# Kernel optimization log

Hardware: AMD Instinct MI355X
Metric: run time of the kernel (lower is better)

Reference implementation:

```python
import jax, jax.numpy as jnp
import numpy as np

N, H, W = 4, 96, 96
C, G, K = 128, 8, 3
GC = C // G          # group channels = 16
P = K * K            # sampling points per group = 9
PAD = K // 2
OFS = 1.0            # offset_scale
HID = 4 * C          # mlp hidden
EPS = 1e-5           # torch nn.LayerNorm default eps


def _ln(x, g, b):
    m = jnp.mean(x, -1, keepdims=True)
    v = jnp.mean((x - m) ** 2, -1, keepdims=True)
    return (x - m) * jax.lax.rsqrt(v + EPS) * g + b


def _dcnv3_core(x, offset, mask):
    # x: (n,H,W,C) channels-last, offset: (n,H,W,G*P*2), mask: (n,H,W,G,P) softmaxed.
    # Faithful port of dcnv3_core_pytorch (stride=1, dilation=1, zero-pad grid_sample,
    # align_corners=False -> pixel = loc*size - 0.5).
    n = x.shape[0]
    xp = jnp.pad(x, ((0, 0), (PAD, PAD), (PAD, PAD), (0, 0)))
    Hin, Win = H + 2 * PAD, W + 2 * PAD
    L = H * W
    base = (K - 1) // 2 + 0.5
    ref_x = (base + jnp.arange(W, dtype=x.dtype)) / Win  # normalized by padded size
    ref_y = (base + jnp.arange(H, dtype=x.dtype)) / Hin
    k = jnp.arange(K, dtype=x.dtype) - (K - 1) // 2
    dx = jnp.repeat(k, K) / Win  # torch meshgrid('ij'): kernel-x varies slowest
    dy = jnp.tile(k, K) / Hin
    off = offset.reshape(n, H, W, G, P, 2)
    # absolute sampling pixel coords (grid_sample align_corners=False)
    px = (ref_x[None, None, :, None, None] + dx * OFS + off[..., 0] * OFS / Win) * Win - 0.5
    py = (ref_y[None, :, None, None, None] + dy * OFS + off[..., 1] * OFS / Hin) * Hin - 0.5
    # layout (n,G,L,P)
    px = px.transpose(0, 3, 1, 2, 4).reshape(n, G, L, P)
    py = py.transpose(0, 3, 1, 2, 4).reshape(n, G, L, P)
    mk = mask.transpose(0, 3, 1, 2, 4).reshape(n, G, L, P)
    xg = xp.reshape(n, Hin * Win, G, GC).transpose(0, 2, 1, 3)
    x0 = jnp.floor(px); y0 = jnp.floor(py)
    fx = px - x0; fy = py - y0
    x0 = x0.astype(jnp.int32); y0 = y0.astype(jnp.int32)
    x1 = x0 + 1; y1 = y0 + 1
    out = jnp.zeros((n, G, L, GC), x.dtype)
    for yi, xi, w in ((y0, x0, (1 - fy) * (1 - fx)), (y0, x1, (1 - fy) * fx),
                      (y1, x0, fy * (1 - fx)), (y1, x1, fy * fx)):
        valid = (yi >= 0) & (yi < Hin) & (xi >= 0) & (xi < Win)
        idx = jnp.clip(yi, 0, Hin - 1) * Win + jnp.clip(xi, 0, Win - 1)
        v = jnp.take_along_axis(xg, idx.reshape(n, G, L * P, 1), axis=2)
        v = v.reshape(n, G, L, P, GC)
        out = out + jnp.einsum('nglp,nglpc->nglc', jnp.where(valid, w, 0.0) * mk, v)
    return out.transpose(0, 2, 1, 3).reshape(n, H, W, C)


def _dcn(x, w_in, b_in, dw_k, dw_b, dwg, dwb, w_off, b_off, w_msk, b_msk, w_out, b_out):
    n = x.shape[0]
    xproj = x @ w_in + b_in
    x1 = jax.lax.conv_general_dilated(
        x, dw_k, (1, 1), 'SAME',
        dimension_numbers=('NHWC', 'HWIO', 'NHWC'),
        feature_group_count=C) + dw_b
    x1 = jax.nn.gelu(_ln(x1, dwg, dwb), approximate=False)
    offset = x1 @ w_off + b_off
    mask = jax.nn.softmax((x1 @ w_msk + b_msk).reshape(n, H, W, G, P), axis=-1)
    y = _dcnv3_core(xproj, offset, mask)
    return y @ w_out + b_out


def setup_inputs() -> dict:
    key = jax.random.key(0)
    ks = jax.random.split(key, 10)
    rn = lambda k, s, sc: jax.random.normal(k, s, jnp.float32) * sc
    return {
        'x': rn(ks[0], (N, H, W, C), 1.0),
        'ln1g': jnp.ones((C,), jnp.float32), 'ln1b': jnp.zeros((C,), jnp.float32),
        'w_in': rn(ks[1], (C, C), 0.02), 'b_in': jnp.zeros((C,), jnp.float32),
        'dw_k': rn(ks[2], (K, K, 1, C), 0.1), 'dw_b': jnp.zeros((C,), jnp.float32),
        'dwg': jnp.ones((C,), jnp.float32), 'dwb': jnp.zeros((C,), jnp.float32),
        'w_off': rn(ks[3], (C, G * P * 2), 0.01), 'b_off': rn(ks[4], (G * P * 2,), 0.1),
        'w_msk': rn(ks[5], (C, G * P), 0.02), 'b_msk': jnp.zeros((G * P,), jnp.float32),
        'w_out': rn(ks[6], (C, C), 0.02), 'b_out': jnp.zeros((C,), jnp.float32),
        'ln2g': jnp.ones((C,), jnp.float32), 'ln2b': jnp.zeros((C,), jnp.float32),
        'w1': rn(ks[7], (C, HID), 0.02), 'b1': jnp.zeros((HID,), jnp.float32),
        'w2': rn(ks[8], (HID, C), 0.02), 'b2': jnp.zeros((C,), jnp.float32),
    }


def reference(x, ln1g, ln1b, w_in, b_in, dw_k, dw_b, dwg, dwb, w_off, b_off,
              w_msk, b_msk, w_out, b_out, ln2g, ln2b, w1, b1, w2, b2):
    # pre-norm InternImage block: x = x + dcn(LN1(x)); x = x + mlp(LN2(x))
    x = x + _dcn(_ln(x, ln1g, ln1b), w_in, b_in, dw_k, dw_b, dwg, dwb,
                 w_off, b_off, w_msk, b_msk, w_out, b_out)
    h = _ln(x, ln2g, ln2b)
    h = jax.nn.gelu(h @ w1 + b1, approximate=False) @ w2 + b2
    return x + h
```

## Files before the change

kernel.cpp:

```cpp
#include <hip/hip_runtime.h>
#include <hip/hip_bf16.h>
#include <math.h>

using bf16 = __hip_bfloat16;
using bf162 = __hip_bfloat162;

typedef __bf16 bf16x8 __attribute__((ext_vector_type(8)));
typedef float floatx4 __attribute__((ext_vector_type(4)));

constexpr int NB = 4, HH = 96, WW = 96, CC = 128, GG = 8, PP = 9;
constexpr int HW = HH * WW;
constexpr int NPIX = NB * HW;

__device__ __forceinline__ float ld1(const float* p) { return *p; }
__device__ __forceinline__ float ld1(const bf16* p)  { return __bfloat162float(*p); }
__device__ __forceinline__ void st1(float* p, float v) { *p = v; }
__device__ __forceinline__ void st1(bf16* p, float v)  { *p = __float2bfloat16(v); }
__device__ __forceinline__ float b2f(bf16 v) { return __bfloat162float(v); }
__device__ __forceinline__ bf16 f2b(float v) { return __float2bfloat16(v); }
__device__ __forceinline__ float gelu_exact(float v) {
    return 0.5f * v * (1.0f + erff(v * 0.7071067811865475f));
}
__device__ __forceinline__ floatx4 MFMA(bf16x8 a, bf16x8 b, floatx4 c) {
    return __builtin_amdgcn_mfma_f32_16x16x32_bf16(a, b, c, 0, 0, 0);
}

struct PrepArgs {
    const float* src[6];
    bf16* dst[6];
    int K[6], N[6];
    int cum[7];
    const float* b_off; const float* b_msk; float* b_om;
};

__global__ __launch_bounds__(256) void prep_weights(PrepArgs pa, int total)
{
    int t = blockIdx.x * 256 + threadIdx.x;
    if (t >= total) return;
    if (t >= pa.cum[6]) {
        int e = t - pa.cum[6];
        pa.b_om[e] = (e < 144) ? pa.b_off[e] : pa.b_msk[e - 144];
        return;
    }
    int i = 0;
    #pragma unroll
    for (int j = 0; j < 5; ++j) if (t >= pa.cum[j + 1]) i = j + 1;
    int e = t - pa.cum[i];
    int Ki = pa.K[i], Ni = pa.N[i];
    int n = e / Ki, k = e - n * Ki;
    pa.dst[i][e] = f2b(pa.src[i][(size_t)k * Ni + n]);
}

template<typename TI, typename TO>
__global__ __launch_bounds__(256) void ln_kernel(
    const TI* __restrict__ X, const float* __restrict__ g,
    const float* __restrict__ b, TO* __restrict__ out)
{
    int wave = (blockIdx.x * 256 + threadIdx.x) >> 6;
    int lane = threadIdx.x & 63;
    if (wave >= NPIX) return;
    const TI* xp = X + (size_t)wave * 128 + 2 * lane;
    float v0 = ld1(xp), v1 = ld1(xp + 1);
    float s = v0 + v1, q = v0 * v0 + v1 * v1;
    #pragma unroll
    for (int o = 32; o; o >>= 1) { s += __shfl_xor(s, o); q += __shfl_xor(q, o); }
    float mean = s * (1.0f / 128.0f);
    float rstd = rsqrtf(q * (1.0f / 128.0f) - mean * mean + 1e-5f);
    float g0 = g[2 * lane], g1 = g[2 * lane + 1];
    float b0 = b[2 * lane], b1 = b[2 * lane + 1];
    TO* op = out + (size_t)wave * 128 + 2 * lane;
    st1(op,     (v0 - mean) * rstd * g0 + b0);
    st1(op + 1, (v1 - mean) * rstd * g1 + b1);
}

__global__ __launch_bounds__(256) void dwconv_ln_gelu_kernel(
    const bf16* __restrict__ xln, const float* __restrict__ dwk,
    const float* __restrict__ dwb, const float* __restrict__ gam,
    const float* __restrict__ bet, bf16* __restrict__ out)
{
    int wave = (blockIdx.x * 256 + threadIdx.x) >> 6;
    int lane = threadIdx.x & 63;
    if (wave >= NPIX) return;
    int n = wave / HW; int rem = wave % HW;
    int y = rem / WW;  int x = rem % WW;
    const bf162* xp = (const bf162*)xln;
    float a0 = 0.f, a1 = 0.f;
    #pragma unroll
    for (int ky = 0; ky < 3; ++ky) {
        int yy = y + ky - 1;
        if (yy < 0 || yy >= HH) continue;
        #pragma unroll
        for (int kx = 0; kx < 3; ++kx) {
            int xx = x + kx - 1;
            if (xx < 0 || xx >= WW) continue;
            bf162 v = xp[((size_t)(n * HH + yy) * WW + xx) * 64 + lane];
            const float* w = dwk + (ky * 3 + kx) * CC + 2 * lane;
            a0 = fmaf(b2f(v.x), w[0], a0);
            a1 = fmaf(b2f(v.y), w[1], a1);
        }
    }
    a0 += dwb[2 * lane]; a1 += dwb[2 * lane + 1];
    float s = a0 + a1, q = a0 * a0 + a1 * a1;
    #pragma unroll
    for (int o = 32; o; o >>= 1) { s += __shfl_xor(s, o); q += __shfl_xor(q, o); }
    float mean = s * (1.0f / 128.0f);
    float rstd = rsqrtf(q * (1.0f / 128.0f) - mean * mean + 1e-5f);
    float h0 = gelu_exact((a0 - mean) * rstd * gam[2 * lane]     + bet[2 * lane]);
    float h1 = gelu_exact((a1 - mean) * rstd * gam[2 * lane + 1] + bet[2 * lane + 1]);
    bf162 o2; o2.x = f2b(h0); o2.y = f2b(h1);
    ((bf162*)out)[(size_t)wave * 64 + lane] = o2;
}

__global__ __launch_bounds__(256) void dcn_core_kernel(
    const bf16* __restrict__ xproj, const bf16* __restrict__ omr,
    bf16* __restrict__ out)
{
    __shared__ int4   sOff[4][72];
    __shared__ float4 sW[4][72];
    __shared__ float  sRaw[4][72];
    int wv = threadIdx.x >> 6;
    int lane = threadIdx.x & 63;
    int pix = blockIdx.x * 4 + wv;
    int n = pix / HW; int rem = pix % HW;
    int iy = rem / WW; int ix = rem % WW;
    const bf16* om = omr + (size_t)pix * 216;

    for (int e = lane; e < 72; e += 64)
        sRaw[wv][e] = b2f(om[144 + e]);
    __syncthreads();

    for (int e = lane; e < 72; e += 64) {
        int g = e / 9, p = e - 9 * g;
        float mx = -1e30f;
        #pragma unroll
        for (int i = 0; i < 9; ++i) mx = fmaxf(mx, sRaw[wv][g * 9 + i]);
        float ssum = 0.f;
        #pragma unroll
        for (int i = 0; i < 9; ++i) ssum += __expf(sRaw[wv][g * 9 + i] - mx);
        float mw = __expf(sRaw[wv][e] - mx) / ssum;

        float ox = b2f(om[g * 18 + 2 * p]);
        float oy = b2f(om[g * 18 + 2 * p + 1]);
        int kx = p / 3 - 1, ky = p % 3 - 1;
        float px = (float)(ix + kx) + ox;
        float py = (float)(iy + ky) + oy;
        float fx0 = floorf(px), fy0 = floorf(py);
        int x0 = (int)fx0, y0 = (int)fy0;
        float fx = px - fx0, fy = py - fy0;
        bool vx0 = (x0 >= 0) & (x0 < WW), vx1 = (x0 + 1 >= 0) & (x0 + 1 < WW);
        bool vy0 = (y0 >= 0) & (y0 < HH), vy1 = (y0 + 1 >= 0) & (y0 + 1 < HH);
        float w00 = (1.f - fy) * (1.f - fx) * mw * (vy0 && vx0 ? 1.f : 0.f);
        float w01 = (1.f - fy) * fx         * mw * (vy0 && vx1 ? 1.f : 0.f);
        float w10 = fy * (1.f - fx)         * mw * (vy1 && vx0 ? 1.f : 0.f);
        float w11 = fy * fx                 * mw * (vy1 && vx1 ? 1.f : 0.f);
        int x0c = min(max(x0, 0), WW - 1), x1c = min(max(x0 + 1, 0), WW - 1);
        int y0c = min(max(y0, 0), HH - 1), y1c = min(max(y0 + 1, 0), HH - 1);
        sOff[wv][e] = make_int4((y0c * WW + x0c) * CC, (y0c * WW + x1c) * CC,
                                (y1c * WW + x0c) * CC, (y1c * WW + x1c) * CC);
        sW[wv][e] = make_float4(w00, w01, w10, w11);
    }
    __syncthreads();

    const bf16* xb = xproj + (size_t)n * HW * CC + 2 * lane;
    int gbase = (lane >> 3) * 9;
    float a0 = 0.f, a1 = 0.f;
    #pragma unroll
    for (int p = 0; p < 9; ++p) {
        int4 o = sOff[wv][gbase + p];
        float4 w = sW[wv][gbase + p];
        bf162 v00 = *(const bf162*)(xb + o.x);
        bf162 v01 = *(const bf162*)(xb + o.y);
        bf162 v10 = *(const bf162*)(xb + o.z);
        bf162 v11 = *(const bf162*)(xb + o.w);
        a0 += w.x * b2f(v00.x) + w.y * b2f(v01.x) + w.z * b2f(v10.x) + w.w * b2f(v11.x);
        a1 += w.x * b2f(v00.y) + w.y * b2f(v01.y) + w.z * b2f(v10.y) + w.w * b2f(v11.y);
    }
    bf162 o2; o2.x = f2b(a0); o2.y = f2b(a1);
    ((bf162*)out)[(size_t)pix * 64 + lane] = o2;
}

__global__ __launch_bounds__(256) void gemm_mfma_kernel(
    const bf16* __restrict__ A, const bf16* __restrict__ Wt,
    const float* __restrict__ bias, bf16* __restrict__ Out, int M, int Nn)
{
    __shared__ __align__(16) __bf16 As[64][136];
    __shared__ __align__(16) __bf16 Bs[64][136];
    int tid = threadIdx.x;
    int wv = tid >> 6, lane = tid & 63;
    int bm = blockIdx.y * 64, bn = blockIdx.x * 64;
    int mI = lane & 15, q = lane >> 4;

    #pragma unroll
    for (int i = 0; i < 4; ++i) {
        int s = tid + 256 * i;
        int row = s >> 4, ko = (s & 15) * 8;
        *reinterpret_cast<uint4*>(&As[row][ko]) =
            *reinterpret_cast<const uint4*>(A + (size_t)(bm + row) * 128 + ko);
        int ng = bn + row;
        uint4 bv = make_uint4(0, 0, 0, 0);
        if (ng < Nn) bv = *reinterpret_cast<const uint4*>(Wt + (size_t)ng * 128 + ko);
        *reinterpret_cast<uint4*>(&Bs[row][ko]) = bv;
    }
    __syncthreads();

    floatx4 acc[4] = {};
    #pragma unroll
    for (int ks = 0; ks < 4; ++ks) {
        int k = ks * 32 + q * 8;
        bf16x8 a = *reinterpret_cast<const bf16x8*>(&As[wv * 16 + mI][k]);
        #pragma unroll
        for (int t = 0; t < 4; ++t) {
            bf16x8 b = *reinterpret_cast<const bf16x8*>(&Bs[t * 16 + mI][k]);
            acc[t] = MFMA(a, b, acc[t]);
        }
    }
    int row0 = bm + wv * 16 + q * 4;
    #pragma unroll
    for (int t = 0; t < 4; ++t) {
        int col = bn + t * 16 + mI;
        if (col >= Nn) continue;
        float bs = bias[col];
        #pragma unroll
        for (int r = 0; r < 4; ++r)
            st1(Out + (size_t)(row0 + r) * Nn + col, acc[t][r] + bs);
    }
}

__global__ __launch_bounds__(256, 3) void fused_tail_kernel(
    const bf16* __restrict__ ycore, const float* __restrict__ x,
    const bf16* __restrict__ w_outT, const float* __restrict__ b_out,
    const float* __restrict__ ln2g, const float* __restrict__ ln2b,
    const bf16* __restrict__ w1T, const float* __restrict__ b1,
    const bf16* __restrict__ w2T, const float* __restrict__ b2,
    float* __restrict__ out)
{
    __shared__ __align__(16) bf16 sA[64 * 136];
    __shared__ __align__(16) bf16 sXres[64 * 136];
    __shared__ __align__(16) bf16 sH2[64 * 136];
    int tid = threadIdx.x, wv = tid >> 6, lane = tid & 63;
    int mI = lane & 15, q = lane >> 4;
    int bm = blockIdx.x * 64;

    bf16x8 bw0[4][2];
    #pragma unroll
    for (int ks = 0; ks < 4; ++ks)
        #pragma unroll
        for (int ct = 0; ct < 2; ++ct)
            bw0[ks][ct] = *reinterpret_cast<const bf16x8*>(
                w_outT + (size_t)(wv * 32 + ct * 16 + mI) * 128 + ks * 32 + q * 8);

    #pragma unroll
    for (int i = 0; i < 4; ++i) {
        int s = tid + 256 * i;
        int row = s >> 4, ko = (s & 15) * 8;
        *reinterpret_cast<uint4*>(&sA[row * 136 + ko]) =
            *reinterpret_cast<const uint4*>(ycore + (size_t)(bm + row) * 128 + ko);
    }
    __syncthreads();

    floatx4 acc0[4][2] = {};
    #pragma unroll
    for (int ks = 0; ks < 4; ++ks) {
        int k = ks * 32 + q * 8;
        bf16x8 a[4];
        #pragma unroll
        for (int rt = 0; rt < 4; ++rt)
            a[rt] = *reinterpret_cast<const bf16x8*>(&sA[(rt * 16 + mI) * 136 + k]);
        #pragma unroll
        for (int ct = 0; ct < 2; ++ct)
            #pragma unroll
            for (int rt = 0; rt < 4; ++rt)
                acc0[rt][ct] = MFMA(a[rt], bw0[ks][ct], acc0[rt][ct]);
    }
    #pragma unroll
    for (int rt = 0; rt < 4; ++rt)
        #pragma unroll
        for (int ct = 0; ct < 2; ++ct) {
            int col = wv * 32 + ct * 16 + mI;
            float bs = b_out[col];
            #pragma unroll
            for (int r = 0; r < 4; ++r) {
                int row = rt * 16 + q * 4 + r;
                float v = acc0[rt][ct][r] + bs + x[(size_t)(bm + row) * 128 + col];
                sXres[row * 136 + col] = f2b(v);
            }
        }
    __syncthreads();

    {
        int row = tid >> 2, part = tid & 3;
        float s = 0.f, sq = 0.f;
        float vals[32];
        #pragma unroll
        for (int j = 0; j < 4; ++j) {
            bf16x8 v = *reinterpret_cast<const bf16x8*>(&sXres[row * 136 + part * 32 + j * 8]);
            #pragma unroll
            for (int e = 0; e < 8; ++e) {
                float f = (float)v[e];
                vals[j * 8 + e] = f; s += f; sq += f * f;
            }
        }
        s  += __shfl_xor(s, 1);  s += __shfl_xor(s, 2);
        sq += __shfl_xor(sq, 1); sq += __shfl_xor(sq, 2);
        float mean = s * (1.0f / 128.0f);
        float rstd = rsqrtf(sq * (1.0f / 128.0f) - mean * mean + 1e-5f);
        #pragma unroll
        for (int j = 0; j < 4; ++j) {
            bf16x8 o;
            #pragma unroll
            for (int e = 0; e < 8; ++e) {
                int ch = part * 32 + j * 8 + e;
                bf16 t = f2b((vals[j * 8 + e] - mean) * rstd * ln2g[ch] + ln2b[ch]);
                o[e] = *reinterpret_cast<__bf16*>(&t);
            }
            *reinterpret_cast<bf16x8*>(&sH2[row * 136 + part * 32 + j * 8]) = o;
        }
    }
    __syncthreads();

    floatx4 acc2[4][2] = {};
    #pragma unroll 1
    for (int ph = 0; ph < 4; ++ph) {
        bf16x8 bw1[4][2];
        #pragma unroll
        for (int ks = 0; ks < 4; ++ks)
            #pragma unroll
            for (int ct = 0; ct < 2; ++ct)
                bw1[ks][ct] = *reinterpret_cast<const bf16x8*>(
                    w1T + (size_t)(ph * 128 + wv * 32 + ct * 16 + mI) * 128 + ks * 32 + q * 8);
        floatx4 acc1[4][2] = {};
        #pragma unroll
        for (int ks = 0; ks < 4; ++ks) {
            int k = ks * 32 + q * 8;
            bf16x8 a[4];
            #pragma unroll
            for (int rt = 0; rt < 4; ++rt)
                a[rt] = *reinterpret_cast<const bf16x8*>(&sH2[(rt * 16 + mI) * 136 + k]);
            #pragma unroll
            for (int ct = 0; ct < 2; ++ct)
                #pragma unroll
                for (int rt = 0; rt < 4; ++rt)
                    acc1[rt][ct] = MFMA(a[rt], bw1[ks][ct], acc1[rt][ct]);
        }
        __syncthreads();
        bf16x8 bw2[4][2];
        #pragma unroll
        for (int ks = 0; ks < 4; ++ks)
            #pragma unroll
            for (int ct = 0; ct < 2; ++ct)
                bw2[ks][ct] = *reinterpret_cast<const bf16x8*>(
                    w2T + (size_t)(wv * 32 + ct * 16 + mI) * 512 + ph * 128 + ks * 32 + q * 8);
        #pragma unroll
        for (int rt = 0; rt < 4; ++rt)
            #pragma unroll
            for (int ct = 0; ct < 2; ++ct) {
                int lcol = wv * 32 + ct * 16 + mI;
                float bs = b1[ph * 128 + lcol];
                #pragma unroll
                for (int r = 0; r < 4; ++r) {
                    int row = rt * 16 + q * 4 + r;
                    sA[row * 136 + lcol] = f2b(gelu_exact(acc1[rt][ct][r] + bs));
                }
            }
        __syncthreads();
        #pragma unroll
        for (int ks = 0; ks < 4; ++ks) {
            int k = ks * 32 + q * 8;
            bf16x8 a[4];
            #pragma unroll
            for (int rt = 0; rt < 4; ++rt)
                a[rt] = *reinterpret_cast<const bf16x8*>(&sA[(rt * 16 + mI) * 136 + k]);
            #pragma unroll
            for (int ct = 0; ct < 2; ++ct)
                #pragma unroll
                for (int rt = 0; rt < 4; ++rt)
                    acc2[rt][ct] = MFMA(a[rt], bw2[ks][ct], acc2[rt][ct]);
        }
    }
    #pragma unroll
    for (int rt = 0; rt < 4; ++rt)
        #pragma unroll
        for (int ct = 0; ct < 2; ++ct) {
            int col = wv * 32 + ct * 16 + mI;
            float bs = b2[col];
            #pragma unroll
            for (int r = 0; r < 4; ++r) {
                int row = rt * 16 + q * 4 + r;
                out[(size_t)(bm + row) * 128 + col] =
                    acc2[rt][ct][r] + bs + b2f(sXres[row * 136 + col]);
            }
        }
}

extern "C" void kernel_launch(void* const* d_in, const int* in_sizes, int n_in,
                              void* d_out, int out_size, void* d_ws, size_t ws_size,
                              hipStream_t stream)
{
    const float* x     = (const float*)d_in[0];
    const float* ln1g  = (const float*)d_in[1];
    const float* ln1b  = (const float*)d_in[2];
    const float* w_in  = (const float*)d_in[3];
    const float* b_in  = (const float*)d_in[4];
    const float* dw_k  = (const float*)d_in[5];
    const float* dw_b  = (const float*)d_in[6];
    const float* dwg   = (const float*)d_in[7];
    const float* dwb   = (const float*)d_in[8];
    const float* w_off = (const float*)d_in[9];
    const float* b_off = (const float*)d_in[10];
    const float* w_msk = (const float*)d_in[11];
    const float* b_msk = (const float*)d_in[12];
    const float* w_out = (const float*)d_in[13];
    const float* b_out = (const float*)d_in[14];
    const float* ln2g  = (const float*)d_in[15];
    const float* ln2b  = (const float*)d_in[16];
    const float* w1    = (const float*)d_in[17];
    const float* b1    = (const float*)d_in[18];
    const float* w2    = (const float*)d_in[19];
    const float* b2    = (const float*)d_in[20];
    float* out = (float*)d_out;

    bf16* ws = (bf16*)d_ws;
    bf16* xln   = ws;
    bf16* xproj = xln   + (size_t)NPIX * 128;
    bf16* x1    = xproj + (size_t)NPIX * 128;
    bf16* omr   = x1    + (size_t)NPIX * 128;
    bf16* ycore = xln;
    bf16* wT    = ws + (size_t)NPIX * 600;
    bf16* w_inT  = wT;
    bf16* w_omT  = w_inT  + 16384;
    bf16* w_outT = w_omT  + 27648;
    bf16* w1T    = w_outT + 16384;
    bf16* w2T    = w1T    + 65536;
    float* b_om  = (float*)(w2T + 65536);
    const int WTOT = 191488 + 216;

    PrepArgs pa;
    pa.src[0] = w_in;  pa.dst[0] = w_inT;            pa.K[0] = 128; pa.N[0] = 128;
    pa.src[1] = w_off; pa.dst[1] = w_omT;            pa.K[1] = 128; pa.N[1] = 144;
    pa.src[2] = w_msk; pa.dst[2] = w_omT + 144*128;  pa.K[2] = 128; pa.N[2] = 72;
    pa.src[3] = w_out; pa.dst[3] = w_outT;           pa.K[3] = 128; pa.N[3] = 128;
    pa.src[4] = w1;    pa.dst[4] = w1T;              pa.K[4] = 128; pa.N[4] = 512;
    pa.src[5] = w2;    pa.dst[5] = w2T;              pa.K[5] = 512; pa.N[5] = 128;
    pa.cum[0] = 0;     pa.cum[1] = 16384;  pa.cum[2] = 34816; pa.cum[3] = 44032;
    pa.cum[4] = 60416; pa.cum[5] = 125952; pa.cum[6] = 191488;
    pa.b_off = b_off;  pa.b_msk = b_msk;   pa.b_om = b_om;

    const int M = NPIX;
    dim3 blk(256);

    prep_weights<<<(WTOT + 255) / 256, blk, 0, stream>>>(pa, WTOT);
    ln_kernel<float, bf16><<<NPIX / 4, blk, 0, stream>>>(x, ln1g, ln1b, xln);
    gemm_mfma_kernel<<<dim3(2, M / 64), blk, 0, stream>>>(
        xln, w_inT, b_in, xproj, M, 128);
    dwconv_ln_gelu_kernel<<<NPIX / 4, blk, 0, stream>>>(xln, dw_k, dw_b, dwg, dwb, x1);
    gemm_mfma_kernel<<<dim3(4, M / 64), blk, 0, stream>>>(
        x1, w_omT, b_om, omr, M, 216);
    dcn_core_kernel<<<NPIX / 4, blk, 0, stream>>>(xproj, omr, ycore);
    fused_tail_kernel<<<M / 64, blk, 0, stream>>>(
        ycore, x, w_outT, b_out, ln2g, ln2b, w1T, b1, w2T, b2, out);
}
```

Before: 238.8 us.

## Merge independent launches into block-partitioned kernels and load GEMM weights into registers

Weight prep and LN1 now run in one launch, with blocks split by index. The input-projection GEMM and the dwconv+LN+GELU kernel share a second launch in the same way, since both only read xln. The GEMM body now loads B weights straight from global into registers instead of staging them through shared memory, and LN1 uses vectorised float2 loads. This cuts two kernel launches and the serialization between independent stages, at the cost of more register pressure and mixed block kinds within one grid.

```diff
diff --git a/kernel.cpp b/kernel.cpp
--- a/kernel.cpp
+++ b/kernel.cpp
@@ -33,34 +33,33 @@
     const float* b_off; const float* b_msk; float* b_om;
 };
 
-__global__ __launch_bounds__(256) void prep_weights(PrepArgs pa, int total)
-{
-    int t = blockIdx.x * 256 + threadIdx.x;
-    if (t >= total) return;
-    if (t >= pa.cum[6]) {
-        int e = t - pa.cum[6];
-        pa.b_om[e] = (e < 144) ? pa.b_off[e] : pa.b_msk[e - 144];
+__global__ __launch_bounds__(256) void k1_prep_ln(
+    PrepArgs pa, int total, int prepBlocks,
+    const float* __restrict__ X, const float* __restrict__ g,
+    const float* __restrict__ b, bf16* __restrict__ xln)
+{
+    if ((int)blockIdx.x < prepBlocks) {
+        int t = blockIdx.x * 256 + threadIdx.x;
+        if (t >= total) return;
+        if (t >= pa.cum[6]) {
+            int e = t - pa.cum[6];
+            pa.b_om[e] = (e < 144) ? pa.b_off[e] : pa.b_msk[e - 144];
+            return;
+        }
+        int i = 0;
+        #pragma unroll
+        for (int j = 0; j < 5; ++j) if (t >= pa.cum[j + 1]) i = j + 1;
+        int e = t - pa.cum[i];
+        int Ki = pa.K[i], Ni = pa.N[i];
+        int n = e / Ki, k = e - n * Ki;
+        pa.dst[i][e] = f2b(pa.src[i][(size_t)k * Ni + n]);
         return;
     }
-    int i = 0;
-    #pragma unroll
-    for (int j = 0; j < 5; ++j) if (t >= pa.cum[j + 1]) i = j + 1;
-    int e = t - pa.cum[i];
-    int Ki = pa.K[i], Ni = pa.N[i];
-    int n = e / Ki, k = e - n * Ki;
-    pa.dst[i][e] = f2b(pa.src[i][(size_t)k * Ni + n]);
-}
-
-template<typename TI, typename TO>
-__global__ __launch_bounds__(256) void ln_kernel(
-    const TI* __restrict__ X, const float* __restrict__ g,
-    const float* __restrict__ b, TO* __restrict__ out)
-{
-    int wave = (blockIdx.x * 256 + threadIdx.x) >> 6;
+    int wave = ((blockIdx.x - prepBlocks) * 256 + threadIdx.x) >> 6;
     int lane = threadIdx.x & 63;
     if (wave >= NPIX) return;
-    const TI* xp = X + (size_t)wave * 128 + 2 * lane;
-    float v0 = ld1(xp), v1 = ld1(xp + 1);
+    float2 v = *reinterpret_cast<const float2*>(X + (size_t)wave * 128 + 2 * lane);
+    float v0 = v.x, v1 = v.y;
     float s = v0 + v1, q = v0 * v0 + v1 * v1;
     #pragma unroll
     for (int o = 32; o; o >>= 1) { s += __shfl_xor(s, o); q += __shfl_xor(q, o); }
@@ -68,18 +67,75 @@
     float rstd = rsqrtf(q * (1.0f / 128.0f) - mean * mean + 1e-5f);
     float g0 = g[2 * lane], g1 = g[2 * lane + 1];
     float b0 = b[2 * lane], b1 = b[2 * lane + 1];
-    TO* op = out + (size_t)wave * 128 + 2 * lane;
-    st1(op,     (v0 - mean) * rstd * g0 + b0);
-    st1(op + 1, (v1 - mean) * rstd * g1 + b1);
-}
-
-__global__ __launch_bounds__(256) void dwconv_ln_gelu_kernel(
-    const bf16* __restrict__ xln, const float* __restrict__ dwk,
-    const float* __restrict__ dwb, const float* __restrict__ gam,
-    const float* __restrict__ bet, bf16* __restrict__ out)
-{
-    int wave = (blockIdx.x * 256 + threadIdx.x) >> 6;
-    int lane = threadIdx.x & 63;
+    bf162 o2; o2.x = f2b((v0 - mean) * rstd * g0 + b0);
+    o2.y = f2b((v1 - mean) * rstd * g1 + b1);
+    ((bf162*)xln)[(size_t)wave * 64 + lane] = o2;
+}
+
+template<int NN>
+__device__ __forceinline__ void gemm_a_body(
+    __bf16 (*As)[136], const bf16* __restrict__ A, const bf16* __restrict__ Wt,
+    const float* __restrict__ bias, bf16* __restrict__ Out, int bm, int bn, int tid)
+{
+    int wv = tid >> 6, lane = tid & 63;
+    int mI = lane & 15, q = lane >> 4;
+    bf16x8 bw[4][4];
+    #pragma unroll
+    for (int t = 0; t < 4; ++t) {
+        int ng = bn + t * 16 + mI;
+        #pragma unroll
+        for (int ks = 0; ks < 4; ++ks) {
+            bf16x8 bv = {};
+            if (NN == 128 || ng < NN)
+                bv = *reinterpret_cast<const bf16x8*>(Wt + (size_t)ng * 128 + ks * 32 + q * 8);
+            bw[t][ks] = bv;
+        }
+    }
+    #pragma unroll
+    for (int i = 0; i < 4; ++i) {
+        int s = tid + 256 * i;
+        int row = s >> 4, ko = (s & 15) * 8;
+        *reinterpret_cast<uint4*>(&As[row][ko]) =
+            *reinterpret_cast<const uint4*>(A + (size_t)(bm + row) * 128 + ko);
+    }
+    __syncthreads();
+    floatx4 acc[4] = {};
+    #pragma unroll
+    for (int ks = 0; ks < 4; ++ks) {
+        int k = ks * 32 + q * 8;
+        bf16x8 a = *reinterpret_cast<const bf16x8*>(&As[wv * 16 + mI][k]);
+        #pragma unroll
+        for (int t = 0; t < 4; ++t)
+            acc[t] = MFMA(a, bw[t][ks], acc[t]);
+    }
+    int row0 = bm + wv * 16 + q * 4;
+    #pragma unroll
+    for (int t = 0; t < 4; ++t) {
+        int col = bn + t * 16 + mI;
+        if (NN != 128 && col >= NN) continue;
+        float bs = bias[col];
+        #pragma unroll
+        for (int r = 0; r < 4; ++r)
+            st1(Out + (size_t)(row0 + r) * NN + col, acc[t][r] + bs);
+    }
+}
+
+__global__ __launch_bounds__(256) void k2_gemm_dwconv(
+    const bf16* __restrict__ xln, const bf16* __restrict__ w_inT,
+    const float* __restrict__ b_in, bf16* __restrict__ xproj,
+    const float* __restrict__ dwk, const float* __restrict__ dwb,
+    const float* __restrict__ gam, const float* __restrict__ bet,
+    bf16* __restrict__ out, int gemmBlocks)
+{
+    __shared__ __align__(16) __bf16 As[64][136];
+    int tid = threadIdx.x;
+    if ((int)blockIdx.x < gemmBlocks) {
+        int bx = blockIdx.x & 1, by = blockIdx.x >> 1;
+        gemm_a_body<128>(As, xln, w_inT, b_in, xproj, by * 64, bx * 64, tid);
+        return;
+    }
+    int wave = ((blockIdx.x - gemmBlocks) * 256 + tid) >> 6;
+    int lane = tid & 63;
     if (wave >= NPIX) return;
     int n = wave / HW; int rem = wave % HW;
     int y = rem / WW;  int x = rem % WW;
@@ -109,6 +165,15 @@
     float h1 = gelu_exact((a1 - mean) * rstd * gam[2 * lane + 1] + bet[2 * lane + 1]);
     bf162 o2; o2.x = f2b(h0); o2.y = f2b(h1);
     ((bf162*)out)[(size_t)wave * 64 + lane] = o2;
+}
+
+__global__ __launch_bounds__(256) void gemm_a_kernel216(
+    const bf16* __restrict__ A, const bf16* __restrict__ Wt,
+    const float* __restrict__ bias, bf16* __restrict__ Out)
+{
+    __shared__ __align__(16) __bf16 As[64][136];
+    gemm_a_body<216>(As, A, Wt, bias, Out, blockIdx.y * 64, blockIdx.x * 64,
+                     threadIdx.x);
 }
 
 __global__ __launch_bounds__(256) void dcn_core_kernel(
@@ -177,53 +242,6 @@
     }
     bf162 o2; o2.x = f2b(a0); o2.y = f2b(a1);
     ((bf162*)out)[(size_t)pix * 64 + lane] = o2;
-}
-
-__global__ __launch_bounds__(256) void gemm_mfma_kernel(
-    const bf16* __restrict__ A, const bf16* __restrict__ Wt,
-    const float* __restrict__ bias, bf16* __restrict__ Out, int M, int Nn)
-{
-    __shared__ __align__(16) __bf16 As[64][136];
-    __shared__ __align__(16) __bf16 Bs[64][136];
-    int tid = threadIdx.x;
-    int wv = tid >> 6, lane = tid & 63;
-    int bm = blockIdx.y * 64, bn = blockIdx.x * 64;
-    int mI = lane & 15, q = lane >> 4;
-
-    #pragma unroll
-    for (int i = 0; i < 4; ++i) {
-        int s = tid + 256 * i;
-        int row = s >> 4, ko = (s & 15) * 8;
-        *reinterpret_cast<uint4*>(&As[row][ko]) =
-            *reinterpret_cast<const uint4*>(A + (size_t)(bm + row) * 128 + ko);
-        int ng = bn + row;
-        uint4 bv = make_uint4(0, 0, 0, 0);
-        if (ng < Nn) bv = *reinterpret_cast<const uint4*>(Wt + (size_t)ng * 128 + ko);
-        *reinterpret_cast<uint4*>(&Bs[row][ko]) = bv;
-    }
-    __syncthreads();
-
-    floatx4 acc[4] = {};
-    #pragma unroll
-    for (int ks = 0; ks < 4; ++ks) {
-        int k = ks * 32 + q * 8;
-        bf16x8 a = *reinterpret_cast<const bf16x8*>(&As[wv * 16 + mI][k]);
-        #pragma unroll
-        for (int t = 0; t < 4; ++t) {
-            bf16x8 b = *reinterpret_cast<const bf16x8*>(&Bs[t * 16 + mI][k]);
-            acc[t] = MFMA(a, b, acc[t]);
-        }
-    }
-    int row0 = bm + wv * 16 + q * 4;
-    #pragma unroll
-    for (int t = 0; t < 4; ++t) {
-        int col = bn + t * 16 + mI;
-        if (col >= Nn) continue;
-        float bs = bias[col];
-        #pragma unroll
-        for (int r = 0; r < 4; ++r)
-            st1(Out + (size_t)(row0 + r) * Nn + col, acc[t][r] + bs);
-    }
 }
 
 __global__ __launch_bounds__(256, 3) void fused_tail_kernel(
@@ -447,14 +465,14 @@
 
     const int M = NPIX;
     dim3 blk(256);
-
-    prep_weights<<<(WTOT + 255) / 256, blk, 0, stream>>>(pa, WTOT);
-    ln_kernel<float, bf16><<<NPIX / 4, blk, 0, stream>>>(x, ln1g, ln1b, xln);
-    gemm_mfma_kernel<<<dim3(2, M / 64), blk, 0, stream>>>(
-        xln, w_inT, b_in, xproj, M, 128);
-    dwconv_ln_gelu_kernel<<<NPIX / 4, blk, 0, stream>>>(xln, dw_k, dw_b, dwg, dwb, x1);
-    gemm_mfma_kernel<<<dim3(4, M / 64), blk, 0, stream>>>(
-        x1, w_omT, b_om, omr, M, 216);
+    const int prepBlocks = (WTOT + 255) / 256;
+    const int gemmBlocks = 2 * (M / 64);
+
+    k1_prep_ln<<<prepBlocks + NPIX / 4, blk, 0, stream>>>(
+        pa, WTOT, prepBlocks, x, ln1g, ln1b, xln);
+    k2_gemm_dwconv<<<gemmBlocks + NPIX / 4, blk, 0, stream>>>(
+        xln, w_inT, b_in, xproj, dw_k, dw_b, dwg, dwb, x1, gemmBlocks);
+    gemm_a_kernel216<<<dim3(4, M / 64), blk, 0, stream>>>(x1, w_omT, b_om, omr);
     dcn_core_kernel<<<NPIX / 4, blk, 0, stream>>>(xproj, omr, ycore);
     fused_tail_kernel<<<M / 64, blk, 0, stream>>>(
         ycore, x, w_outT, b_out, ln2g, ln2b, w1T, b1, w2T, b2, out);
```

Measured after the change: 255.1 us. 6.8% more time.

## Fuse offset/mask projection GEMM into the deformable sampling kernel

Applied to the files above, without the earlier changes.

Replaces the separate offset/mask GEMM launch and the DCN core kernel with one kernel. Each block computes the 216-wide offset/mask projection for 16 pixels with MFMA into shared memory, then does softmax, bilinear weighting and gathering per pixel. This removes the global write and re-read of the offset/mask intermediate and one kernel launch. In exchange, every block reads the projection weights from global memory (relying on L2), the MFMA step runs at low utilisation on 16-row tiles, and the per-wave shared scratch is reused across pixels with no explicit barrier.

```diff
diff --git a/kernel.cpp b/kernel.cpp
--- a/kernel.cpp
+++ b/kernel.cpp
@@ -109,74 +109,6 @@
     float h1 = gelu_exact((a1 - mean) * rstd * gam[2 * lane + 1] + bet[2 * lane + 1]);
     bf162 o2; o2.x = f2b(h0); o2.y = f2b(h1);
     ((bf162*)out)[(size_t)wave * 64 + lane] = o2;
-}
-
-__global__ __launch_bounds__(256) void dcn_core_kernel(
-    const bf16* __restrict__ xproj, const bf16* __restrict__ omr,
-    bf16* __restrict__ out)
-{
-    __shared__ int4   sOff[4][72];
-    __shared__ float4 sW[4][72];
-    __shared__ float  sRaw[4][72];
-    int wv = threadIdx.x >> 6;
-    int lane = threadIdx.x & 63;
-    int pix = blockIdx.x * 4 + wv;
-    int n = pix / HW; int rem = pix % HW;
-    int iy = rem / WW; int ix = rem % WW;
-    const bf16* om = omr + (size_t)pix * 216;
-
-    for (int e = lane; e < 72; e += 64)
-        sRaw[wv][e] = b2f(om[144 + e]);
-    __syncthreads();
-
-    for (int e = lane; e < 72; e += 64) {
-        int g = e / 9, p = e - 9 * g;
-        float mx = -1e30f;
-        #pragma unroll
-        for (int i = 0; i < 9; ++i) mx = fmaxf(mx, sRaw[wv][g * 9 + i]);
-        float ssum = 0.f;
-        #pragma unroll
-        for (int i = 0; i < 9; ++i) ssum += __expf(sRaw[wv][g * 9 + i] - mx);
-        float mw = __expf(sRaw[wv][e] - mx) / ssum;
-
-        float ox = b2f(om[g * 18 + 2 * p]);
-        float oy = b2f(om[g * 18 + 2 * p + 1]);
-        int kx = p / 3 - 1, ky = p % 3 - 1;
-        float px = (float)(ix + kx) + ox;
-        float py = (float)(iy + ky) + oy;
-        float fx0 = floorf(px), fy0 = floorf(py);
-        int x0 = (int)fx0, y0 = (int)fy0;
-        float fx = px - fx0, fy = py - fy0;
-        bool vx0 = (x0 >= 0) & (x0 < WW), vx1 = (x0 + 1 >= 0) & (x0 + 1 < WW);
-        bool vy0 = (y0 >= 0) & (y0 < HH), vy1 = (y0 + 1 >= 0) & (y0 + 1 < HH);
-        float w00 = (1.f - fy) * (1.f - fx) * mw * (vy0 && vx0 ? 1.f : 0.f);
-        float w01 = (1.f - fy) * fx         * mw * (vy0 && vx1 ? 1.f : 0.f);
-        float w10 = fy * (1.f - fx)         * mw * (vy1 && vx0 ? 1.f : 0.f);
-        float w11 = fy * fx                 * mw * (vy1 && vx1 ? 1.f : 0.f);
-        int x0c = min(max(x0, 0), WW - 1), x1c = min(max(x0 + 1, 0), WW - 1);
-        int y0c = min(max(y0, 0), HH - 1), y1c = min(max(y0 + 1, 0), HH - 1);
-        sOff[wv][e] = make_int4((y0c * WW + x0c) * CC, (y0c * WW + x1c) * CC,
-                                (y1c * WW + x0c) * CC, (y1c * WW + x1c) * CC);
-        sW[wv][e] = make_float4(w00, w01, w10, w11);
-    }
-    __syncthreads();
-
-    const bf16* xb = xproj + (size_t)n * HW * CC + 2 * lane;
-    int gbase = (lane >> 3) * 9;
-    float a0 = 0.f, a1 = 0.f;
-    #pragma unroll
-    for (int p = 0; p < 9; ++p) {
-        int4 o = sOff[wv][gbase + p];
-        float4 w = sW[wv][gbase + p];
-        bf162 v00 = *(const bf162*)(xb + o.x);
-        bf162 v01 = *(const bf162*)(xb + o.y);
-        bf162 v10 = *(const bf162*)(xb + o.z);
-        bf162 v11 = *(const bf162*)(xb + o.w);
-        a0 += w.x * b2f(v00.x) + w.y * b2f(v01.x) + w.z * b2f(v10.x) + w.w * b2f(v11.x);
-        a1 += w.x * b2f(v00.y) + w.y * b2f(v01.y) + w.z * b2f(v10.y) + w.w * b2f(v11.y);
-    }
-    bf162 o2; o2.x = f2b(a0); o2.y = f2b(a1);
-    ((bf162*)out)[(size_t)pix * 64 + lane] = o2;
 }
 
 __global__ __launch_bounds__(256) void gemm_mfma_kernel(
@@ -223,6 +155,109 @@
         #pragma unroll
         for (int r = 0; r < 4; ++r)
             st1(Out + (size_t)(row0 + r) * Nn + col, acc[t][r] + bs);
+    }
+}
+
+constexpr int SOMR = 228;
+__global__ __launch_bounds__(256) void dcn_fused_kernel(
+    const bf16* __restrict__ xproj, const bf16* __restrict__ x1,
+    const bf16* __restrict__ w_omT, const float* __restrict__ b_om,
+    bf16* __restrict__ out)
+{
+    __shared__ __align__(16) __bf16 sX1[16][136];
+    __shared__ __align__(16) __bf16 sOmr[16][SOMR];
+    __shared__ int4   sOff[4][72];
+    __shared__ float4 sW[4][72];
+    int tid = threadIdx.x, wv = tid >> 6, lane = tid & 63;
+    int mI = lane & 15, q = lane >> 4;
+    int bp = blockIdx.x * 16;
+
+    {
+        int row = tid >> 4, ko = (tid & 15) * 8;
+        *reinterpret_cast<uint4*>(&sX1[row][ko]) =
+            *reinterpret_cast<const uint4*>(x1 + (size_t)(bp + row) * 128 + ko);
+    }
+    __syncthreads();
+
+    {
+        bf16x8 a[4];
+        #pragma unroll
+        for (int ks = 0; ks < 4; ++ks)
+            a[ks] = *reinterpret_cast<const bf16x8*>(&sX1[mI][ks * 32 + q * 8]);
+        for (int t = wv; t < 14; t += 4) {
+            int ng = t * 16 + mI;
+            floatx4 acc = {};
+            #pragma unroll
+            for (int ks = 0; ks < 4; ++ks) {
+                bf16x8 b = {};
+                if (ng < 216)
+                    b = *reinterpret_cast<const bf16x8*>(
+                        w_omT + (size_t)ng * 128 + ks * 32 + q * 8);
+                acc = MFMA(a[ks], b, acc);
+            }
+            float bs = (ng < 216) ? b_om[ng] : 0.f;
+            #pragma unroll
+            for (int r = 0; r < 4; ++r)
+                sOmr[q * 4 + r][ng] = *(__bf16*)&(const bf16&)f2b(acc[r] + bs);
+        }
+    }
+    __syncthreads();
+
+    for (int pp = 0; pp < 4; ++pp) {
+        int pr = wv * 4 + pp;
+        int pix = bp + pr;
+        int n = pix / HW; int rem = pix % HW;
+        int iy = rem / WW; int ix = rem % WW;
+
+        for (int e = lane; e < 72; e += 64) {
+            int g = e / 9, p = e - 9 * g;
+            float mx = -1e30f;
+            #pragma unroll
+            for (int i = 0; i < 9; ++i)
+                mx = fmaxf(mx, b2f(*(const bf16*)&sOmr[pr][144 + g * 9 + i]));
+            float ssum = 0.f;
+            #pragma unroll
+            for (int i = 0; i < 9; ++i)
+                ssum += __expf(b2f(*(const bf16*)&sOmr[pr][144 + g * 9 + i]) - mx);
+            float mw = __expf(b2f(*(const bf16*)&sOmr[pr][144 + e]) - mx) / ssum;
+
+            float ox = b2f(*(const bf16*)&sOmr[pr][g * 18 + 2 * p]);
+            float oy = b2f(*(const bf16*)&sOmr[pr][g * 18 + 2 * p + 1]);
+            int kx = p / 3 - 1, ky = p % 3 - 1;
+            float px = (float)(ix + kx) + ox;
+            float py = (float)(iy + ky) + oy;
+            float fx0 = floorf(px), fy0 = floorf(py);
+            int x0 = (int)fx0, y0 = (int)fy0;
+            float fx = px - fx0, fy = py - fy0;
+            bool vx0 = (x0 >= 0) & (x0 < WW), vx1 = (x0 + 1 >= 0) & (x0 + 1 < WW);
+            bool vy0 = (y0 >= 0) & (y0 < HH), vy1 = (y0 + 1 >= 0) & (y0 + 1 < HH);
+            float w00 = (1.f - fy) * (1.f - fx) * mw * (vy0 && vx0 ? 1.f : 0.f);
+            float w01 = (1.f - fy) * fx         * mw * (vy0 && vx1 ? 1.f : 0.f);
+            float w10 = fy * (1.f - fx)         * mw * (vy1 && vx0 ? 1.f : 0.f);
+            float w11 = fy * fx                 * mw * (vy1 && vx1 ? 1.f : 0.f);
+            int x0c = min(max(x0, 0), WW - 1), x1c = min(max(x0 + 1, 0), WW - 1);
+            int y0c = min(max(y0, 0), HH - 1), y1c = min(max(y0 + 1, 0), HH - 1);
+            sOff[wv][e] = make_int4((y0c * WW + x0c) * CC, (y0c * WW + x1c) * CC,
+                                    (y1c * WW + x0c) * CC, (y1c * WW + x1c) * CC);
+            sW[wv][e] = make_float4(w00, w01, w10, w11);
+        }
+
+        const bf16* xb = xproj + (size_t)n * HW * CC + 2 * lane;
+        int gbase = (lane >> 3) * 9;
+        float a0 = 0.f, a1 = 0.f;
+        #pragma unroll
+        for (int p = 0; p < 9; ++p) {
+            int4 o = sOff[wv][gbase + p];
+            float4 w = sW[wv][gbase + p];
+            bf162 v00 = *(const bf162*)(xb + o.x);
+            bf162 v01 = *(const bf162*)(xb + o.y);
+            bf162 v10 = *(const bf162*)(xb + o.z);
+            bf162 v11 = *(const bf162*)(xb + o.w);
+            a0 += w.x * b2f(v00.x) + w.y * b2f(v01.x) + w.z * b2f(v10.x) + w.w * b2f(v11.x);
+            a1 += w.x * b2f(v00.y) + w.y * b2f(v01.y) + w.z * b2f(v10.y) + w.w * b2f(v11.y);
+        }
+        bf162 o2; o2.x = f2b(a0); o2.y = f2b(a1);
+        ((bf162*)out)[(size_t)pix * 64 + lane] = o2;
     }
 }
 
@@ -423,7 +458,6 @@
     bf16* xln   = ws;
     bf16* xproj = xln   + (size_t)NPIX * 128;
     bf16* x1    = xproj + (size_t)NPIX * 128;
-    bf16* omr   = x1    + (size_t)NPIX * 128;
     bf16* ycore = xln;
     bf16* wT    = ws + (size_t)NPIX * 600;
     bf16* w_inT  = wT;
@@ -453,9 +487,7 @@
     gemm_mfma_kernel<<<dim3(2, M / 64), blk, 0, stream>>>(
         xln, w_inT, b_in, xproj, M, 128);
     dwconv_ln_gelu_kernel<<<NPIX / 4, blk, 0, stream>>>(xln, dw_k, dw_b, dwg, dwb, x1);
-    gemm_mfma_kernel<<<dim3(4, M / 64), blk, 0, stream>>>(
-        x1, w_omT, b_om, omr, M, 216);
-    dcn_core_kernel<<<NPIX / 4, blk, 0, stream>>>(xproj, omr, ycore);
+    dcn_fused_kernel<<<NPIX / 16, blk, 0, stream>>>(xproj, x1, w_omT, b_om, ycore);
     fused_tail_kernel<<<M / 64, blk, 0, stream>>>(
         ycore, x, w_outT, b_out, ln2g, ln2b, w1T, b1, w2T, b2, out);
 }
```

Result: no change. 235.4 us (-1.4%).
